# Kernel optimization log

Measured on AMD Instinct MI355X. Metric: run time of the kernel, lower is better.

The kernel has to match this reference:

```python
import jax, jax.numpy as jnp
import numpy as np

B, S, D = 2, 2048, 1024
H, HD = 16, 64          # n_heads, head_dim
FF, HID = 4096, 8192    # d_ff, swiglu hidden (= 2*d_ff)


def _ln(x, eps=1e-5):
    # non-parametric LayerNorm (fp8_layernorm_noparam in source)
    m = jnp.mean(x, axis=-1, keepdims=True)
    v = jnp.var(x, axis=-1, keepdims=True)
    return (x - m) * jax.lax.rsqrt(v + eps)


def setup_inputs() -> dict:
    key = jax.random.key(0)
    ks = jax.random.split(key, 7)
    s = 0.02  # init std
    return {
        "x": jax.random.normal(ks[0], (B, S, D), jnp.float32),
        "Wq": jax.random.normal(ks[1], (D, D), jnp.float32) * s,
        "Wk": jax.random.normal(ks[2], (D, D), jnp.float32) * s,
        "Wv": jax.random.normal(ks[3], (D, D), jnp.float32) * s,
        "Wo": jax.random.normal(ks[4], (D, D), jnp.float32) * s,
        "Wff": jax.random.normal(ks[5], (HID, D), jnp.float32) * s,
        "Wout": jax.random.normal(ks[6], (FF, D), jnp.float32).T * s,  # [D, FF] -> stored as Linear weight [D_out=D, D_in=FF]
    }


def reference(x, Wq, Wk, Wv, Wo, Wff, Wout):
    b, s, d = x.shape
    # attention sub-block
    h = _ln(x)
    q = (h @ Wq.T).reshape(b, s, H, HD).transpose(0, 2, 1, 3)  # [B,H,S,HD]
    k = (h @ Wk.T).reshape(b, s, H, HD).transpose(0, 2, 1, 3)
    v = (h @ Wv.T).reshape(b, s, H, HD).transpose(0, 2, 1, 3)
    scale = 1.0 / float(HD) ** 0.5
    scores = jnp.einsum('bhqd,bhkd->bhqk', q, k) * scale        # [B,H,S,S] naive full matrix
    causal = jnp.tril(jnp.ones((s, s), dtype=bool))
    scores = jnp.where(causal, scores, jnp.finfo(scores.dtype).min)
    attn = jax.nn.softmax(scores, axis=-1)
    att = jnp.einsum('bhqk,bhkd->bhqd', attn, v)                # [B,H,S,HD]
    att = att.transpose(0, 2, 1, 3).reshape(b, s, d)
    x = x + att @ Wo.T
    # MLP sub-block (SwiGLU, OLMo Llama-style)
    h2 = _ln(x)
    ff = h2 @ Wff.T                                             # [B,S,HID]
    x1, x2 = jnp.split(ff, 2, axis=-1)
    g = jax.nn.silu(x1) * x2                                    # [B,S,FF]
    return x + g @ Wout.T
```

## Files before the change

### kernel.cpp

```cpp
#include <hip/hip_runtime.h>
#include <hip/hip_bf16.h>

#define B_ 2
#define S_ 2048
#define D_ 1024
#define H_ 16
#define FF_ 4096
#define M_ (B_*S_)

using u16 = unsigned short;
using u32 = unsigned int;
typedef __attribute__((ext_vector_type(8))) short short8;
typedef __attribute__((ext_vector_type(4))) float f32x4;
typedef __attribute__((ext_vector_type(16))) float f32x16;
typedef __attribute__((ext_vector_type(4))) unsigned short u16x4;
typedef __attribute__((ext_vector_type(4))) unsigned int u32x4;

static __device__ __forceinline__ u16 f2bf(float f) {
  __hip_bfloat16 h = __float2bfloat16(f);
  return *reinterpret_cast<u16*>(&h);
}
static __device__ __forceinline__ float bf2f(u16 u) {
  __hip_bfloat16 h; *reinterpret_cast<u16*>(&h) = u;
  return __bfloat162float(h);
}

#define GLDS(gp, lp) __builtin_amdgcn_global_load_lds( \
    (const __attribute__((address_space(1))) void*)(gp), \
    (__attribute__((address_space(3))) void*)(lp), 16, 0, 0)

#define MFMA16(a, b, c) __builtin_amdgcn_mfma_f32_16x16x32_bf16(a, b, c, 0, 0, 0)
#define VMC(n) asm volatile("s_waitcnt vmcnt(" #n ")" ::: "memory")
#define BAR() __builtin_amdgcn_s_barrier()

__global__ __launch_bounds__(256) void conv_f32_bf16(
    const float* __restrict__ src, u16* __restrict__ dst, int n4) {
  int i = blockIdx.x * 256 + threadIdx.x;
  if (i < n4) {
    float4 v = reinterpret_cast<const float4*>(src)[i];
    u16x4 o;
    o.x = f2bf(v.x); o.y = f2bf(v.y); o.z = f2bf(v.z); o.w = f2bf(v.w);
    reinterpret_cast<u16x4*>(dst)[i] = o;
  }
}

__global__ __launch_bounds__(256) void ln_rows(
    const float* __restrict__ x, u16* __restrict__ out) {
  int row = blockIdx.x;
  int t = threadIdx.x;
  float4 v = reinterpret_cast<const float4*>(x + (size_t)row * D_)[t];
  float s  = v.x + v.y + v.z + v.w;
  float ss = v.x*v.x + v.y*v.y + v.z*v.z + v.w*v.w;
  #pragma unroll
  for (int off = 1; off < 64; off <<= 1) {
    s  += __shfl_xor(s,  off, 64);
    ss += __shfl_xor(ss, off, 64);
  }
  __shared__ float rs[4], rss[4];
  int wid = t >> 6;
  if ((t & 63) == 0) { rs[wid] = s; rss[wid] = ss; }
  __syncthreads();
  s  = rs[0] + rs[1] + rs[2] + rs[3];
  ss = rss[0] + rss[1] + rss[2] + rss[3];
  float mean = s * (1.0f / D_);
  float var  = ss * (1.0f / D_) - mean * mean;
  float r = rsqrtf(var + 1e-5f);
  u16x4 o;
  o.x = f2bf((v.x - mean) * r);
  o.y = f2bf((v.y - mean) * r);
  o.z = f2bf((v.z - mean) * r);
  o.w = f2bf((v.w - mean) * r);
  reinterpret_cast<u16x4*>(out + (size_t)row * D_)[t] = o;
}

template<int MODE>
__global__ __launch_bounds__(256, 2) void gemm_bt2(
    const u16* __restrict__ A, const u16* __restrict__ W,
    void* __restrict__ C, const u16* __restrict__ aux,
    const float* __restrict__ res, int M, int N, int K)
{
  __shared__ u16 lds[32768];
  const int tid = threadIdx.x;
  const int wid = tid >> 6, lane = tid & 63;
  const int g = lane >> 4, c = lane & 15;
  const int gridN = N >> 7;
  int nwg = gridDim.x;
  int lin = blockIdx.x;
  lin = (lin & 7) * (nwg >> 3) + (lin >> 3);
  const int bm = lin / gridN, bn = lin % gridN;
  const int wm = wid >> 1, wn = wid & 1;
  const int NT = K >> 6;

  f32x4 acc[4][4];
  #pragma unroll
  for (int i = 0; i < 4; i++)
    #pragma unroll
    for (int j = 0; j < 4; j++) acc[i][j] = {0.f, 0.f, 0.f, 0.f};

  auto stage = [&](int sel, int t) {
    const u16* src = sel ? W : A;
    const int tilerow = (sel ? bn : bm) * 128;
    char* dst = (char*)&lds[sel * 16384 + (t & 1) * 8192];
    #pragma unroll
    for (int i = 0; i < 4; i++) {
      int j = i * 256 + tid;
      int row = j >> 3, col16 = j & 7;
      const u16* gp = src + (size_t)(tilerow + row) * K + t * 64 + ((col16 ^ (row & 7)) << 3);
      GLDS(gp, dst + j * 16);
    }
  };

  stage(0, 0); stage(1, 0);
  __syncthreads();

  for (int t = 0; t < NT; t++) {
    const int buf = t & 1;
    if (t + 1 < NT) { stage(0, t + 1); stage(1, t + 1); }

    short8 af[2][4], bfr[2][4];
    #pragma unroll
    for (int ks = 0; ks < 2; ks++)
      #pragma unroll
      for (int m = 0; m < 4; m++) {
        int rh = wm * 64 + m * 16 + c;
        af[ks][m] = *reinterpret_cast<const short8*>(
            &lds[buf * 8192 + rh * 64 + ((((ks << 2) | g) ^ (rh & 7)) << 3)]);
      }
    #pragma unroll
    for (int ks = 0; ks < 2; ks++)
      #pragma unroll
      for (int n = 0; n < 4; n++) {
        int rh = wn * 64 + n * 16 + c;
        bfr[ks][n] = *reinterpret_cast<const short8*>(
            &lds[16384 + buf * 8192 + rh * 64 + ((((ks << 2) | g) ^ (rh & 7)) << 3)]);
      }
    __builtin_amdgcn_s_setprio(1);
    #pragma unroll
    for (int m = 0; m < 4; m++)
      #pragma unroll
      for (int n = 0; n < 4; n++) {
        acc[m][n] = MFMA16(af[0][m], bfr[0][n], acc[m][n]);
        acc[m][n] = MFMA16(af[1][m], bfr[1][n], acc[m][n]);
      }
    __builtin_amdgcn_s_setprio(0);
    __syncthreads();
  }

  #pragma unroll
  for (int m = 0; m < 4; m++)
    #pragma unroll
    for (int n = 0; n < 4; n++)
      #pragma unroll
      for (int r = 0; r < 4; r++) {
        int gr = bm * 128 + wm * 64 + m * 16 + g * 4 + r;
        int gc = bn * 128 + wn * 64 + n * 16 + c;
        size_t idx = (size_t)gr * N + gc;
        float v = acc[m][n][r];
        if (MODE == 0) {
          ((u16*)C)[idx] = f2bf(v);
        } else if (MODE == 1) {
          ((float*)C)[idx] = v + res[idx];
        }
      }
}

__global__ __launch_bounds__(256, 2) void gemm_ff(
    const u16* __restrict__ A, const u16* __restrict__ W,
    u16* __restrict__ Cout, int M, int N, int K)
{
  __shared__ u16 lds[24576];
  const int tid = threadIdx.x;
  const int wid = tid >> 6, lane = tid & 63;
  const int g = lane >> 4, c = lane & 15;
  const int gridN = N >> 7;
  int nwg = gridDim.x;
  int lin = blockIdx.x;
  lin = (lin & 7) * (nwg >> 3) + (lin >> 3);
  const int bm = lin / gridN, bn = lin % gridN;
  const int wm = wid >> 1, wn = wid & 1;
  const int NT = K >> 5;

  f32x4 ac1[4][4], ac2[4][4];
  #pragma unroll
  for (int i = 0; i < 4; i++)
    #pragma unroll
    for (int j = 0; j < 4; j++) { ac1[i][j] = {0.f,0.f,0.f,0.f}; ac2[i][j] = {0.f,0.f,0.f,0.f}; }

  auto stage = [&](int sel, int t) {
    const u16* src = (sel == 0) ? A : W;
    const int rowbase = (sel == 0) ? bm * 128 : (sel == 1 ? bn * 128 : 4096 + bn * 128);
    char* dst = (char*)&lds[sel * 8192 + (t & 1) * 4096];
    #pragma unroll
    for (int i = 0; i < 2; i++) {
      int j = i * 256 + tid;
      int r = j >> 2, cslot = j & 3;
      int csrc = cslot ^ ((r >> 1) & 3);
      const u16* gp = src + (size_t)(rowbase + r) * K + t * 32 + csrc * 8;
      GLDS(gp, dst + j * 16);
    }
  };

  stage(0, 0); stage(1, 0); stage(2, 0);
  __syncthreads();

  for (int t = 0; t < NT; t++) {
    const int buf = t & 1;
    if (t + 1 < NT) { stage(0, t + 1); stage(1, t + 1); stage(2, t + 1); }

    short8 af[4], b1f[4], b2f[4];
    #pragma unroll
    for (int m = 0; m < 4; m++) {
      int rh = wm * 64 + m * 16 + c;
      af[m] = *reinterpret_cast<const short8*>(
          &lds[buf * 4096 + rh * 32 + ((g ^ ((rh >> 1) & 3)) << 3)]);
    }
    #pragma unroll
    for (int n = 0; n < 4; n++) {
      int rh = wn * 64 + n * 16 + c;
      b1f[n] = *reinterpret_cast<const short8*>(
          &lds[8192 + buf * 4096 + rh * 32 + ((g ^ ((rh >> 1) & 3)) << 3)]);
      b2f[n] = *reinterpret_cast<const short8*>(
          &lds[16384 + buf * 4096 + rh * 32 + ((g ^ ((rh >> 1) & 3)) << 3)]);
    }
    __builtin_amdgcn_s_setprio(1);
    #pragma unroll
    for (int m = 0; m < 4; m++)
      #pragma unroll
      for (int n = 0; n < 4; n++) {
        ac1[m][n] = MFMA16(af[m], b1f[n], ac1[m][n]);
        ac2[m][n] = MFMA16(af[m], b2f[n], ac2[m][n]);
      }
    __builtin_amdgcn_s_setprio(0);
    __syncthreads();
  }

  #pragma unroll
  for (int m = 0; m < 4; m++)
    #pragma unroll
    for (int n = 0; n < 4; n++)
      #pragma unroll
      for (int r = 0; r < 4; r++) {
        int gr = bm * 128 + wm * 64 + m * 16 + g * 4 + r;
        int gc = bn * 128 + wn * 64 + n * 16 + c;
        float v1 = ac1[m][n][r];
        float v2 = ac2[m][n][r];
        float gv = (v1 / (1.0f + __expf(-v1))) * v2;
        Cout[(size_t)gr * N + gc] = f2bf(gv);
      }
}

__global__ __launch_bounds__(256) void transpose_v(
    const u16* __restrict__ qkv, u16* __restrict__ vT) {
  __shared__ u16 t[64][66];
  int bh = blockIdx.y;
  int s0 = blockIdx.x * 64;
  int b = bh >> 4, h = bh & 15;
  int tid = threadIdx.x;
  #pragma unroll
  for (int it = 0; it < 2; it++) {
    int idx = it * 256 + tid;
    int row = idx >> 3;
    int cc  = (idx & 7) * 8;
    const u16* src = qkv + ((size_t)(b * S_ + s0 + row)) * 3072 + 2048 + h * 64 + cc;
    short8 v = *reinterpret_cast<const short8*>(src);
    #pragma unroll
    for (int j = 0; j < 8; j++) t[row][cc + j] = (u16)v[j];
  }
  __syncthreads();
  #pragma unroll
  for (int it = 0; it < 2; it++) {
    int idx = it * 256 + tid;
    int d  = idx >> 3;
    int sc = (idx & 7) * 8;
    short8 o;
    #pragma unroll
    for (int j = 0; j < 8; j++) o[j] = (short)t[sc + j][d];
    *reinterpret_cast<short8*>(vT + ((size_t)bh * 64 + d) * S_ + s0 + sc) = o;
  }
}

__global__ __launch_bounds__(256) void attn_split(
    const u16* __restrict__ qkv, const u16* __restrict__ vT,
    u16* __restrict__ pO, float* __restrict__ pML) {
  __shared__ u16 Kl[2][2048];
  __shared__ u16 Vl[2][2048];
  const int tid  = threadIdx.x;
  const int lane = tid & 63;
  const int wid  = tid >> 6;
  const int l31  = lane & 31;
  const int half = lane >> 5;

  int lin = blockIdx.x;
  int swz = (lin & 7) * 160 + (lin >> 3);
  int bh  = swz / 40;
  int j   = swz - bh * 40;
  int qq = 15, rem = j;
  while (rem > (qq >> 2)) { rem -= (qq >> 2) + 1; qq--; }
  int ci = rem;
  const int qt  = qq * 4 + wid;
  const int kt0 = ci * 16;
  const int nt  = min(qq * 4 + 3, kt0 + 15) - kt0;
  int ubase = (qt < 16) ? qt : (qt < 32) ? 16 + (qt - 16) * 2 + ci
            : (qt < 48) ? 48 + (qt - 32) * 3 + ci : 96 + (qt - 48) * 4 + ci;
  const int punit = bh * 160 + ubase;

  const int b = bh >> 4, hd = bh & 15;
  const int q_base = qt * 32;

  const u16* Qb = qkv + ((size_t)(b * S_ + q_base + l31)) * 3072 + hd * 64;
  const u16* Kb = qkv + (size_t)b * S_ * 3072 + 1024 + hd * 64;
  const u16* Vt = vT + (size_t)bh * 64 * S_;

  short8 qf[4];
  #pragma unroll
  for (int dt = 0; dt < 4; dt++) {
    short8 v = *reinterpret_cast<const short8*>(Qb + dt * 16 + half * 8);
    #pragma unroll
    for (int jj = 0; jj < 8; jj++) v[jj] = (short)f2bf(bf2f((u16)v[jj]) * 0.18033688f);
    qf[dt] = v;
  }

  auto stageKV = [&](int kt, int buf) {
    {
      int row = tid >> 3, cs = tid & 7;
      int c = cs ^ (row & 7);
      const u16* gp = Kb + (size_t)(kt * 32 + row) * 3072 + c * 8;
      GLDS(gp, (char*)&Kl[buf][0] + tid * 16);
    }
    {
      int row = tid >> 2, cs = tid & 3;
      int c = cs ^ (row & 3);
      const u16* gp = Vt + (size_t)row * S_ + kt * 32 + c * 8;
      GLDS(gp, (char*)&Vl[buf][0] + tid * 16);
    }
  };

  f32x16 o0, o1;
  #pragma unroll
  for (int r = 0; r < 16; r++) { o0[r] = 0.f; o1[r] = 0.f; }
  float m = -1e30f, lsum = 0.f;

  stageKV(kt0, 0);
  VMC(0); BAR();

  for (int i = 0; ; i++) {
    const int kt = kt0 + i;
    const int buf = i & 1;
    if (i < nt) stageKV(kt + 1, buf ^ 1);

    if (kt <= qt) {
      const bool diag = (kt == qt);
      short8 kfr[4], vfr[4];
      #pragma unroll
      for (int dt = 0; dt < 4; dt++) {
        int cs = (dt * 2 + half) ^ (l31 & 7);
        kfr[dt] = *reinterpret_cast<const short8*>((const char*)&Kl[buf][0] + l31 * 128 + cs * 16);
      }
      {
        int r0 = l31, r1 = 32 + l31;
        vfr[0] = *reinterpret_cast<const short8*>((const char*)&Vl[buf][0] + r0 * 64 + ((half       ^ (r0 & 3)) * 16));
        vfr[1] = *reinterpret_cast<const short8*>((const char*)&Vl[buf][0] + r0 * 64 + (((2 + half) ^ (r0 & 3)) * 16));
        vfr[2] = *reinterpret_cast<const short8*>((const char*)&Vl[buf][0] + r1 * 64 + ((half       ^ (r1 & 3)) * 16));
        vfr[3] = *reinterpret_cast<const short8*>((const char*)&Vl[buf][0] + r1 * 64 + (((2 + half) ^ (r1 & 3)) * 16));
      }

      f32x16 s;
      #pragma unroll
      for (int r = 0; r < 16; r++) s[r] = 0.f;
      __builtin_amdgcn_s_setprio(1);
      #pragma unroll
      for (int dt = 0; dt < 4; dt++)
        s = __builtin_amdgcn_mfma_f32_32x32x16_bf16(kfr[dt], qf[dt], s, 0, 0, 0);
      __builtin_amdgcn_s_setprio(0);

      float p[16];
      #pragma unroll
      for (int r = 0; r < 16; r++) {
        p[r] = s[r];
        if (diag) {
          int kloc = half * 4 + (r & 3) + 8 * (r >> 2);
          if (kloc > l31) p[r] = -1e30f;
        }
      }
      float t8[8];
      #pragma unroll
      for (int r = 0; r < 8; r++) t8[r] = fmaxf(p[r], p[r + 8]);
      float t4a = fmaxf(t8[0], t8[4]), t4b = fmaxf(t8[1], t8[5]);
      float t4c = fmaxf(t8[2], t8[6]), t4d = fmaxf(t8[3], t8[7]);
      float rm = fmaxf(fmaxf(t4a, t4b), fmaxf(t4c, t4d));
      rm = fmaxf(rm, __shfl_xor(rm, 32, 64));

      if (__any(rm > m + 11.0f)) {
        float mn = fmaxf(m, rm);
        float alpha = exp2f(m - mn);
        m = mn;
        lsum *= alpha;
        #pragma unroll
        for (int r = 0; r < 16; r++) {
          int row = (r & 3) + 8 * (r >> 2) + 4 * half;
          float ar = __shfl(alpha, row, 64);
          o0[r] *= ar; o1[r] *= ar;
        }
      }
      float rs = 0.f;
      #pragma unroll
      for (int r = 0; r < 16; r++) { p[r] = exp2f(p[r] - m); rs += p[r]; }
      rs += __shfl_xor(rs, 32, 64);
      lsum += rs;

      u32 pk[8], sp[8];
      #pragma unroll
      for (int ii = 0; ii < 8; ii++) {
        pk[ii] = (u32)f2bf(p[2 * ii]) | ((u32)f2bf(p[2 * ii + 1]) << 16);
        sp[ii] = (u32)__shfl_xor((int)pk[ii], 32, 64);
      }
      u32x4 a0 = { half ? sp[2] : pk[0], half ? sp[3] : pk[1],
                   half ? pk[2] : sp[0], half ? pk[3] : sp[1] };
      u32x4 a1 = { half ? sp[6] : pk[4], half ? sp[7] : pk[5],
                   half ? pk[6] : sp[4], half ? pk[7] : sp[5] };
      short8 pa0 = *reinterpret_cast<short8*>(&a0);
      short8 pa1 = *reinterpret_cast<short8*>(&a1);

      __builtin_amdgcn_s_setprio(1);
      o0 = __builtin_amdgcn_mfma_f32_32x32x16_bf16(pa0, vfr[0], o0, 0, 0, 0);
      o0 = __builtin_amdgcn_mfma_f32_32x32x16_bf16(pa1, vfr[1], o0, 0, 0, 0);
      o1 = __builtin_amdgcn_mfma_f32_32x32x16_bf16(pa0, vfr[2], o1, 0, 0, 0);
      o1 = __builtin_amdgcn_mfma_f32_32x32x16_bf16(pa1, vfr[3], o1, 0, 0, 0);
      __builtin_amdgcn_s_setprio(0);
    }

    if (i == nt) break;
    VMC(0); BAR();
  }

  #pragma unroll
  for (int r = 0; r < 16; r++) {
    int row = (r & 3) + 8 * (r >> 2) + 4 * half;
    pO[(size_t)punit * 2048 + row * 64 + l31]      = f2bf(o0[r]);
    pO[(size_t)punit * 2048 + row * 64 + 32 + l31] = f2bf(o1[r]);
  }
  if (half == 0) {
    pML[punit * 64 + l31]      = m;
    pML[punit * 64 + 32 + l31] = lsum;
  }
}

__global__ __launch_bounds__(256) void attn_combine(
    const u16* __restrict__ pO, const float* __restrict__ pML,
    u16* __restrict__ att) {
  int gw = blockIdx.x;
  int bh = gw >> 6, qt = gw & 63;
  int b = bh >> 4, hd = bh & 15;
  int nc = (qt >> 4) + 1;
  int base = (qt < 16) ? qt : (qt < 32) ? 16 + (qt - 16) * 2
           : (qt < 48) ? 48 + (qt - 32) * 3 : 96 + (qt - 48) * 4;
  int p0 = bh * 160 + base;
  int q  = threadIdx.x >> 3;
  int d  = (threadIdx.x & 7) * 8;

  float m0 = pML[p0 * 64 + q];
  float l0 = pML[p0 * 64 + 32 + q];
  float m1 = nc > 1 ? pML[(p0 + 1) * 64 + q]      : -1e30f;
  float l1 = nc > 1 ? pML[(p0 + 1) * 64 + 32 + q] : 0.f;
  float m2 = nc > 2 ? pML[(p0 + 2) * 64 + q]      : -1e30f;
  float l2 = nc > 2 ? pML[(p0 + 2) * 64 + 32 + q] : 0.f;
  float m3 = nc > 3 ? pML[(p0 + 3) * 64 + q]      : -1e30f;
  float l3 = nc > 3 ? pML[(p0 + 3) * 64 + 32 + q] : 0.f;
  float M = fmaxf(fmaxf(m0, m1), fmaxf(m2, m3));
  float w0 = exp2f(m0 - M), w1 = exp2f(m1 - M);
  float w2 = exp2f(m2 - M), w3 = exp2f(m3 - M);
  float L = l0 * w0 + l1 * w1 + l2 * w2 + l3 * w3;
  float invL = 1.0f / L;

  float o[8];
  short8 v0 = *reinterpret_cast<const short8*>(&pO[(size_t)p0 * 2048 + q * 64 + d]);
  #pragma unroll
  for (int jj = 0; jj < 8; jj++) o[jj] = bf2f((u16)v0[jj]) * w0;
  if (nc > 1) {
    short8 v = *reinterpret_cast<const short8*>(&pO[(size_t)(p0 + 1) * 2048 + q * 64 + d]);
    #pragma unroll
    for (int jj = 0; jj < 8; jj++) o[jj] += bf2f((u16)v[jj]) * w1;
  }
  if (nc > 2) {
    short8 v = *reinterpret_cast<const short8*>(&pO[(size_t)(p0 + 2) * 2048 + q * 64 + d]);
    #pragma unroll
    for (int jj = 0; jj < 8; jj++) o[jj] += bf2f((u16)v[jj]) * w2;
  }
  if (nc > 3) {
    short8 v = *reinterpret_cast<const short8*>(&pO[(size_t)(p0 + 3) * 2048 + q * 64 + d]);
    #pragma unroll
    for (int jj = 0; jj < 8; jj++) o[jj] += bf2f((u16)v[jj]) * w3;
  }
  short8 ov;
  #pragma unroll
  for (int jj = 0; jj < 8; jj++) ov[jj] = (short)f2bf(o[jj] * invL);
  *reinterpret_cast<short8*>(
      &att[((size_t)(b * S_ + qt * 32 + q)) * D_ + hd * 64 + d]) = ov;
}

extern "C" void kernel_launch(void* const* d_in, const int* in_sizes, int n_in,
                              void* d_out, int out_size, void* d_ws, size_t ws_size,
                              hipStream_t stream) {
  (void)in_sizes; (void)n_in; (void)out_size; (void)ws_size;
  const float* x    = (const float*)d_in[0];
  const float* Wq   = (const float*)d_in[1];
  const float* Wk   = (const float*)d_in[2];
  const float* Wv   = (const float*)d_in[3];
  const float* Wo   = (const float*)d_in[4];
  const float* Wff  = (const float*)d_in[5];
  const float* Wout = (const float*)d_in[6];
  float* out = (float*)d_out;

  char* ws = (char*)d_ws;
  u16*   wqkv = (u16*)(ws);
  u16*   wo   = (u16*)(ws + 6291456);
  u16*   wff  = (u16*)(ws + 8388608);
  u16*   wout = (u16*)(ws + 25165824);
  float* x1   = (float*)(ws + 33554432);
  char*  P    = ws + 50331648;
  u16*   hbuf = (u16*)(P);
  u16*   qkv  = (u16*)(P + 8388608);
  u16*   vT   = (u16*)(P + 33554432);
  u16*   att  = (u16*)(P + 41943040);
  u16*   pO   = (u16*)(P + 50331648);
  float* pML  = (float*)(P + 71303168);
  u16*   h2   = (u16*)(P);
  u16*   gbuf = (u16*)(P + 41943040);

  conv_f32_bf16<<<1024, 256, 0, stream>>>(Wq, wqkv,               262144);
  conv_f32_bf16<<<1024, 256, 0, stream>>>(Wk, wqkv + 1048576,     262144);
  conv_f32_bf16<<<1024, 256, 0, stream>>>(Wv, wqkv + 2097152,     262144);
  conv_f32_bf16<<<1024, 256, 0, stream>>>(Wo, wo,                 262144);
  conv_f32_bf16<<<8192, 256, 0, stream>>>(Wff, wff,               2097152);
  conv_f32_bf16<<<4096, 256, 0, stream>>>(Wout, wout,             1048576);

  ln_rows<<<M_, 256, 0, stream>>>(x, hbuf);
  gemm_bt2<0><<<dim3(768), 256, 0, stream>>>(hbuf, wqkv, qkv, nullptr, nullptr, M_, 3072, 1024);
  transpose_v<<<dim3(32, 32), 256, 0, stream>>>(qkv, vT);
  attn_split<<<dim3(1280), 256, 0, stream>>>(qkv, vT, pO, pML);
  attn_combine<<<dim3(2048), 256, 0, stream>>>(pO, pML, att);
  gemm_bt2<1><<<dim3(256), 256, 0, stream>>>(att, wo, x1, nullptr, x, M_, 1024, 1024);

  ln_rows<<<M_, 256, 0, stream>>>(x1, h2);
  gemm_ff<<<dim3(1024), 256, 0, stream>>>(h2, wff, gbuf, M_, 4096, 1024);
  gemm_bt2<1><<<dim3(256), 256, 0, stream>>>(gbuf, wout, out, nullptr, x1, M_, 1024, 4096);
}
```

Baseline: 281.8 us.

## Triple-buffer GEMM pipelines with single barrier and smaller M tiles for N=1024 GEMMs

After: 298.1 us. 1.06x slower.

```diff
diff --git a/kernel.cpp b/kernel.cpp
--- a/kernel.cpp
+++ b/kernel.cpp
@@ -32,6 +32,7 @@
 #define MFMA16(a, b, c) __builtin_amdgcn_mfma_f32_16x16x32_bf16(a, b, c, 0, 0, 0)
 #define VMC(n) asm volatile("s_waitcnt vmcnt(" #n ")" ::: "memory")
 #define BAR() __builtin_amdgcn_s_barrier()
+#define CFENCE() asm volatile("" ::: "memory")
 
 __global__ __launch_bounds__(256) void conv_f32_bf16(
     const float* __restrict__ src, u16* __restrict__ dst, int n4) {
@@ -73,102 +74,12 @@
   reinterpret_cast<u16x4*>(out + (size_t)row * D_)[t] = o;
 }
 
-template<int MODE>
-__global__ __launch_bounds__(256, 2) void gemm_bt2(
+template<int MODE, int MB>
+__global__ __launch_bounds__(256, 3) void gemm_bt3(
     const u16* __restrict__ A, const u16* __restrict__ W,
-    void* __restrict__ C, const u16* __restrict__ aux,
-    const float* __restrict__ res, int M, int N, int K)
+    void* __restrict__ C, const float* __restrict__ res, int M, int N, int K)
 {
-  __shared__ u16 lds[32768];
-  const int tid = threadIdx.x;
-  const int wid = tid >> 6, lane = tid & 63;
-  const int g = lane >> 4, c = lane & 15;
-  const int gridN = N >> 7;
-  int nwg = gridDim.x;
-  int lin = blockIdx.x;
-  lin = (lin & 7) * (nwg >> 3) + (lin >> 3);
-  const int bm = lin / gridN, bn = lin % gridN;
-  const int wm = wid >> 1, wn = wid & 1;
-  const int NT = K >> 6;
-
-  f32x4 acc[4][4];
-  #pragma unroll
-  for (int i = 0; i < 4; i++)
-    #pragma unroll
-    for (int j = 0; j < 4; j++) acc[i][j] = {0.f, 0.f, 0.f, 0.f};
-
-  auto stage = [&](int sel, int t) {
-    const u16* src = sel ? W : A;
-    const int tilerow = (sel ? bn : bm) * 128;
-    char* dst = (char*)&lds[sel * 16384 + (t & 1) * 8192];
-    #pragma unroll
-    for (int i = 0; i < 4; i++) {
-      int j = i * 256 + tid;
-      int row = j >> 3, col16 = j & 7;
-      const u16* gp = src + (size_t)(tilerow + row) * K + t * 64 + ((col16 ^ (row & 7)) << 3);
-      GLDS(gp, dst + j * 16);
-    }
-  };
-
-  stage(0, 0); stage(1, 0);
-  __syncthreads();
-
-  for (int t = 0; t < NT; t++) {
-    const int buf = t & 1;
-    if (t + 1 < NT) { stage(0, t + 1); stage(1, t + 1); }
-
-    short8 af[2][4], bfr[2][4];
-    #pragma unroll
-    for (int ks = 0; ks < 2; ks++)
-      #pragma unroll
-      for (int m = 0; m < 4; m++) {
-        int rh = wm * 64 + m * 16 + c;
-        af[ks][m] = *reinterpret_cast<const short8*>(
-            &lds[buf * 8192 + rh * 64 + ((((ks << 2) | g) ^ (rh & 7)) << 3)]);
-      }
-    #pragma unroll
-    for (int ks = 0; ks < 2; ks++)
-      #pragma unroll
-      for (int n = 0; n < 4; n++) {
-        int rh = wn * 64 + n * 16 + c;
-        bfr[ks][n] = *reinterpret_cast<const short8*>(
-            &lds[16384 + buf * 8192 + rh * 64 + ((((ks << 2) | g) ^ (rh & 7)) << 3)]);
-      }
-    __builtin_amdgcn_s_setprio(1);
-    #pragma unroll
-    for (int m = 0; m < 4; m++)
-      #pragma unroll
-      for (int n = 0; n < 4; n++) {
-        acc[m][n] = MFMA16(af[0][m], bfr[0][n], acc[m][n]);
-        acc[m][n] = MFMA16(af[1][m], bfr[1][n], acc[m][n]);
-      }
-    __builtin_amdgcn_s_setprio(0);
-    __syncthreads();
-  }
-
-  #pragma unroll
-  for (int m = 0; m < 4; m++)
-    #pragma unroll
-    for (int n = 0; n < 4; n++)
-      #pragma unroll
-      for (int r = 0; r < 4; r++) {
-        int gr = bm * 128 + wm * 64 + m * 16 + g * 4 + r;
-        int gc = bn * 128 + wn * 64 + n * 16 + c;
-        size_t idx = (size_t)gr * N + gc;
-        float v = acc[m][n][r];
-        if (MODE == 0) {
-          ((u16*)C)[idx] = f2bf(v);
-        } else if (MODE == 1) {
-          ((float*)C)[idx] = v + res[idx];
-        }
-      }
-}
-
-__global__ __launch_bounds__(256, 2) void gemm_ff(
-    const u16* __restrict__ A, const u16* __restrict__ W,
-    u16* __restrict__ Cout, int M, int N, int K)
-{
-  __shared__ u16 lds[24576];
+  __shared__ u16 lds[MB * 96 + 12288];
   const int tid = threadIdx.x;
   const int wid = tid >> 6, lane = tid & 63;
   const int g = lane >> 4, c = lane & 15;
@@ -180,33 +91,127 @@
   const int wm = wid >> 1, wn = wid & 1;
   const int NT = K >> 5;
 
-  f32x4 ac1[4][4], ac2[4][4];
-  #pragma unroll
-  for (int i = 0; i < 4; i++)
-    #pragma unroll
-    for (int j = 0; j < 4; j++) { ac1[i][j] = {0.f,0.f,0.f,0.f}; ac2[i][j] = {0.f,0.f,0.f,0.f}; }
-
-  auto stage = [&](int sel, int t) {
-    const u16* src = (sel == 0) ? A : W;
-    const int rowbase = (sel == 0) ? bm * 128 : (sel == 1 ? bn * 128 : 4096 + bn * 128);
-    char* dst = (char*)&lds[sel * 8192 + (t & 1) * 4096];
+  f32x4 acc[MB / 32][4];
+  #pragma unroll
+  for (int i = 0; i < MB / 32; i++)
+    #pragma unroll
+    for (int j = 0; j < 4; j++) acc[i][j] = {0.f, 0.f, 0.f, 0.f};
+
+  auto stage = [&](int t) {
+    #pragma unroll
+    for (int i = 0; i < MB / 64; i++) {
+      int j = i * 256 + tid;
+      int r = j >> 2, cslot = j & 3;
+      const u16* gp = A + (size_t)(bm * MB + r) * K + t * 32 + ((cslot ^ ((r >> 1) & 3)) * 8);
+      GLDS(gp, (char*)&lds[(t % 3) * MB * 32] + j * 16);
+    }
     #pragma unroll
     for (int i = 0; i < 2; i++) {
       int j = i * 256 + tid;
       int r = j >> 2, cslot = j & 3;
-      int csrc = cslot ^ ((r >> 1) & 3);
-      const u16* gp = src + (size_t)(rowbase + r) * K + t * 32 + csrc * 8;
-      GLDS(gp, dst + j * 16);
+      const u16* gp = W + (size_t)(bn * 128 + r) * K + t * 32 + ((cslot ^ ((r >> 1) & 3)) * 8);
+      GLDS(gp, (char*)&lds[MB * 96 + (t % 3) * 4096] + j * 16);
     }
   };
 
-  stage(0, 0); stage(1, 0); stage(2, 0);
-  __syncthreads();
+  stage(0); stage(1);
 
   for (int t = 0; t < NT; t++) {
-    const int buf = t & 1;
-    if (t + 1 < NT) { stage(0, t + 1); stage(1, t + 1); stage(2, t + 1); }
-
+    if (t + 1 < NT) {
+      if constexpr (MB == 128) { VMC(4); } else { VMC(3); }
+    } else {
+      VMC(0);
+    }
+    BAR(); CFENCE();
+    if (t + 2 < NT) stage(t + 2);
+
+    const int buf = t % 3;
+    short8 af[MB / 32], bfr[4];
+    #pragma unroll
+    for (int m = 0; m < MB / 32; m++) {
+      int rh = wm * (MB / 2) + m * 16 + c;
+      af[m] = *reinterpret_cast<const short8*>(
+          &lds[buf * MB * 32 + rh * 32 + ((g ^ ((rh >> 1) & 3)) << 3)]);
+    }
+    #pragma unroll
+    for (int n = 0; n < 4; n++) {
+      int rh = wn * 64 + n * 16 + c;
+      bfr[n] = *reinterpret_cast<const short8*>(
+          &lds[MB * 96 + buf * 4096 + rh * 32 + ((g ^ ((rh >> 1) & 3)) << 3)]);
+    }
+    __builtin_amdgcn_s_setprio(1);
+    #pragma unroll
+    for (int m = 0; m < MB / 32; m++)
+      #pragma unroll
+      for (int n = 0; n < 4; n++)
+        acc[m][n] = MFMA16(af[m], bfr[n], acc[m][n]);
+    __builtin_amdgcn_s_setprio(0);
+  }
+
+  #pragma unroll
+  for (int m = 0; m < MB / 32; m++)
+    #pragma unroll
+    for (int n = 0; n < 4; n++)
+      #pragma unroll
+      for (int r = 0; r < 4; r++) {
+        int gr = bm * MB + wm * (MB / 2) + m * 16 + g * 4 + r;
+        int gc = bn * 128 + wn * 64 + n * 16 + c;
+        size_t idx = (size_t)gr * N + gc;
+        float v = acc[m][n][r];
+        if (MODE == 0) {
+          ((u16*)C)[idx] = f2bf(v);
+        } else {
+          ((float*)C)[idx] = v + res[idx];
+        }
+      }
+}
+
+__global__ __launch_bounds__(256, 2) void gemm_ff(
+    const u16* __restrict__ A, const u16* __restrict__ W,
+    u16* __restrict__ Cout, int M, int N, int K)
+{
+  __shared__ u16 lds[36864];
+  const int tid = threadIdx.x;
+  const int wid = tid >> 6, lane = tid & 63;
+  const int g = lane >> 4, c = lane & 15;
+  const int gridN = N >> 7;
+  int nwg = gridDim.x;
+  int lin = blockIdx.x;
+  lin = (lin & 7) * (nwg >> 3) + (lin >> 3);
+  const int bm = lin / gridN, bn = lin % gridN;
+  const int wm = wid >> 1, wn = wid & 1;
+  const int NT = K >> 5;
+
+  f32x4 ac1[4][4], ac2[4][4];
+  #pragma unroll
+  for (int i = 0; i < 4; i++)
+    #pragma unroll
+    for (int j = 0; j < 4; j++) { ac1[i][j] = {0.f,0.f,0.f,0.f}; ac2[i][j] = {0.f,0.f,0.f,0.f}; }
+
+  auto stage = [&](int t) {
+    #pragma unroll
+    for (int sel = 0; sel < 3; sel++) {
+      const u16* src = (sel == 0) ? A : W;
+      const int rowbase = (sel == 0) ? bm * 128 : (sel == 1 ? bn * 128 : 4096 + bn * 128);
+      char* dst = (char*)&lds[sel * 12288 + (t % 3) * 4096];
+      #pragma unroll
+      for (int i = 0; i < 2; i++) {
+        int j = i * 256 + tid;
+        int r = j >> 2, cslot = j & 3;
+        const u16* gp = src + (size_t)(rowbase + r) * K + t * 32 + ((cslot ^ ((r >> 1) & 3)) * 8);
+        GLDS(gp, dst + j * 16);
+      }
+    }
+  };
+
+  stage(0); stage(1);
+
+  for (int t = 0; t < NT; t++) {
+    if (t + 1 < NT) { VMC(6); } else { VMC(0); }
+    BAR(); CFENCE();
+    if (t + 2 < NT) stage(t + 2);
+
+    const int buf = t % 3;
     short8 af[4], b1f[4], b2f[4];
     #pragma unroll
     for (int m = 0; m < 4; m++) {
@@ -218,9 +223,9 @@
     for (int n = 0; n < 4; n++) {
       int rh = wn * 64 + n * 16 + c;
       b1f[n] = *reinterpret_cast<const short8*>(
-          &lds[8192 + buf * 4096 + rh * 32 + ((g ^ ((rh >> 1) & 3)) << 3)]);
+          &lds[12288 + buf * 4096 + rh * 32 + ((g ^ ((rh >> 1) & 3)) << 3)]);
       b2f[n] = *reinterpret_cast<const short8*>(
-          &lds[16384 + buf * 4096 + rh * 32 + ((g ^ ((rh >> 1) & 3)) << 3)]);
+          &lds[24576 + buf * 4096 + rh * 32 + ((g ^ ((rh >> 1) & 3)) << 3)]);
     }
     __builtin_amdgcn_s_setprio(1);
     #pragma unroll
@@ -231,7 +236,6 @@
         ac2[m][n] = MFMA16(af[m], b2f[n], ac2[m][n]);
       }
     __builtin_amdgcn_s_setprio(0);
-    __syncthreads();
   }
 
   #pragma unroll
@@ -535,13 +539,13 @@
   conv_f32_bf16<<<4096, 256, 0, stream>>>(Wout, wout,             1048576);
 
   ln_rows<<<M_, 256, 0, stream>>>(x, hbuf);
-  gemm_bt2<0><<<dim3(768), 256, 0, stream>>>(hbuf, wqkv, qkv, nullptr, nullptr, M_, 3072, 1024);
+  gemm_bt3<0, 128><<<dim3(768), 256, 0, stream>>>(hbuf, wqkv, qkv, nullptr, M_, 3072, 1024);
   transpose_v<<<dim3(32, 32), 256, 0, stream>>>(qkv, vT);
   attn_split<<<dim3(1280), 256, 0, stream>>>(qkv, vT, pO, pML);
   attn_combine<<<dim3(2048), 256, 0, stream>>>(pO, pML, att);
-  gemm_bt2<1><<<dim3(256), 256, 0, stream>>>(att, wo, x1, nullptr, x, M_, 1024, 1024);
+  gemm_bt3<1, 64><<<dim3(512), 256, 0, stream>>>(att, wo, x1, x, M_, 1024, 1024);
 
   ln_rows<<<M_, 256, 0, stream>>>(x1, h2);
   gemm_ff<<<dim3(1024), 256, 0, stream>>>(h2, wff, gbuf, M_, 4096, 1024);
-  gemm_bt2<1><<<dim3(256), 256, 0, stream>>>(gbuf, wout, out, nullptr, x1, M_, 1024, 4096);
-}
+  gemm_bt3<1, 64><<<dim3(512), 256, 0, stream>>>(gbuf, wout, out, x1, M_, 1024, 4096);
+}
```

## Triple-buffer LDS staging in SwiGLU GEMM and attention with single barrier

Applied to the files above, without the earlier changes.

Result: no change. 286.3 us (+1.6%).

```diff
diff --git a/kernel.cpp b/kernel.cpp
--- a/kernel.cpp
+++ b/kernel.cpp
@@ -32,6 +32,7 @@
 #define MFMA16(a, b, c) __builtin_amdgcn_mfma_f32_16x16x32_bf16(a, b, c, 0, 0, 0)
 #define VMC(n) asm volatile("s_waitcnt vmcnt(" #n ")" ::: "memory")
 #define BAR() __builtin_amdgcn_s_barrier()
+#define CFENCE() asm volatile("" ::: "memory")
 
 __global__ __launch_bounds__(256) void conv_f32_bf16(
     const float* __restrict__ src, u16* __restrict__ dst, int n4) {
@@ -76,8 +77,7 @@
 template<int MODE>
 __global__ __launch_bounds__(256, 2) void gemm_bt2(
     const u16* __restrict__ A, const u16* __restrict__ W,
-    void* __restrict__ C, const u16* __restrict__ aux,
-    const float* __restrict__ res, int M, int N, int K)
+    void* __restrict__ C, const float* __restrict__ res, int M, int N, int K)
 {
   __shared__ u16 lds[32768];
   const int tid = threadIdx.x;
@@ -158,7 +158,7 @@
         float v = acc[m][n][r];
         if (MODE == 0) {
           ((u16*)C)[idx] = f2bf(v);
-        } else if (MODE == 1) {
+        } else {
           ((float*)C)[idx] = v + res[idx];
         }
       }
@@ -168,7 +168,7 @@
     const u16* __restrict__ A, const u16* __restrict__ W,
     u16* __restrict__ Cout, int M, int N, int K)
 {
-  __shared__ u16 lds[24576];
+  __shared__ u16 lds[36864];
   const int tid = threadIdx.x;
   const int wid = tid >> 6, lane = tid & 63;
   const int g = lane >> 4, c = lane & 15;
@@ -186,27 +186,30 @@
     #pragma unroll
     for (int j = 0; j < 4; j++) { ac1[i][j] = {0.f,0.f,0.f,0.f}; ac2[i][j] = {0.f,0.f,0.f,0.f}; }
 
-  auto stage = [&](int sel, int t) {
-    const u16* src = (sel == 0) ? A : W;
-    const int rowbase = (sel == 0) ? bm * 128 : (sel == 1 ? bn * 128 : 4096 + bn * 128);
-    char* dst = (char*)&lds[sel * 8192 + (t & 1) * 4096];
-    #pragma unroll
-    for (int i = 0; i < 2; i++) {
-      int j = i * 256 + tid;
-      int r = j >> 2, cslot = j & 3;
-      int csrc = cslot ^ ((r >> 1) & 3);
-      const u16* gp = src + (size_t)(rowbase + r) * K + t * 32 + csrc * 8;
-      GLDS(gp, dst + j * 16);
+  auto stage = [&](int t) {
+    #pragma unroll
+    for (int sel = 0; sel < 3; sel++) {
+      const u16* src = (sel == 0) ? A : W;
+      const int rowbase = (sel == 0) ? bm * 128 : (sel == 1 ? bn * 128 : 4096 + bn * 128);
+      char* dst = (char*)&lds[sel * 12288 + (t % 3) * 4096];
+      #pragma unroll
+      for (int i = 0; i < 2; i++) {
+        int j = i * 256 + tid;
+        int r = j >> 2, cslot = j & 3;
+        const u16* gp = src + (size_t)(rowbase + r) * K + t * 32 + ((cslot ^ ((r >> 1) & 3)) * 8);
+        GLDS(gp, dst + j * 16);
+      }
     }
   };
 
-  stage(0, 0); stage(1, 0); stage(2, 0);
-  __syncthreads();
+  stage(0); stage(1);
 
   for (int t = 0; t < NT; t++) {
-    const int buf = t & 1;
-    if (t + 1 < NT) { stage(0, t + 1); stage(1, t + 1); stage(2, t + 1); }
-
+    if (t + 1 < NT) { VMC(6); } else { VMC(0); }
+    BAR(); CFENCE();
+    if (t + 2 < NT) stage(t + 2);
+
+    const int buf = t % 3;
     short8 af[4], b1f[4], b2f[4];
     #pragma unroll
     for (int m = 0; m < 4; m++) {
@@ -218,9 +221,9 @@
     for (int n = 0; n < 4; n++) {
       int rh = wn * 64 + n * 16 + c;
       b1f[n] = *reinterpret_cast<const short8*>(
-          &lds[8192 + buf * 4096 + rh * 32 + ((g ^ ((rh >> 1) & 3)) << 3)]);
+          &lds[12288 + buf * 4096 + rh * 32 + ((g ^ ((rh >> 1) & 3)) << 3)]);
       b2f[n] = *reinterpret_cast<const short8*>(
-          &lds[16384 + buf * 4096 + rh * 32 + ((g ^ ((rh >> 1) & 3)) << 3)]);
+          &lds[24576 + buf * 4096 + rh * 32 + ((g ^ ((rh >> 1) & 3)) << 3)]);
     }
     __builtin_amdgcn_s_setprio(1);
     #pragma unroll
@@ -231,7 +234,6 @@
         ac2[m][n] = MFMA16(af[m], b2f[n], ac2[m][n]);
       }
     __builtin_amdgcn_s_setprio(0);
-    __syncthreads();
   }
 
   #pragma unroll
@@ -282,8 +284,8 @@
 __global__ __launch_bounds__(256) void attn_split(
     const u16* __restrict__ qkv, const u16* __restrict__ vT,
     u16* __restrict__ pO, float* __restrict__ pML) {
-  __shared__ u16 Kl[2][2048];
-  __shared__ u16 Vl[2][2048];
+  __shared__ u16 Kl[3][2048];
+  __shared__ u16 Vl[3][2048];
   const int tid  = threadIdx.x;
   const int lane = tid & 63;
   const int wid  = tid >> 6;
@@ -329,7 +331,7 @@
     }
     {
       int row = tid >> 2, cs = tid & 3;
-      int c = cs ^ (row & 3);
+      int c = cs ^ ((row >> 1) & 3);
       const u16* gp = Vt + (size_t)row * S_ + kt * 32 + c * 8;
       GLDS(gp, (char*)&Vl[buf][0] + tid * 16);
     }
@@ -341,12 +343,13 @@
   float m = -1e30f, lsum = 0.f;
 
   stageKV(kt0, 0);
-  VMC(0); BAR();
+  if (nt >= 1) { stageKV(kt0 + 1, 1); VMC(2); } else { VMC(0); }
+  BAR();
 
   for (int i = 0; ; i++) {
     const int kt = kt0 + i;
-    const int buf = i & 1;
-    if (i < nt) stageKV(kt + 1, buf ^ 1);
+    const int buf = i % 3;
+    if (i + 2 <= nt) stageKV(kt0 + i + 2, (i + 2) % 3);
 
     if (kt <= qt) {
       const bool diag = (kt == qt);
@@ -358,10 +361,11 @@
       }
       {
         int r0 = l31, r1 = 32 + l31;
-        vfr[0] = *reinterpret_cast<const short8*>((const char*)&Vl[buf][0] + r0 * 64 + ((half       ^ (r0 & 3)) * 16));
-        vfr[1] = *reinterpret_cast<const short8*>((const char*)&Vl[buf][0] + r0 * 64 + (((2 + half) ^ (r0 & 3)) * 16));
-        vfr[2] = *reinterpret_cast<const short8*>((const char*)&Vl[buf][0] + r1 * 64 + ((half       ^ (r1 & 3)) * 16));
-        vfr[3] = *reinterpret_cast<const short8*>((const char*)&Vl[buf][0] + r1 * 64 + (((2 + half) ^ (r1 & 3)) * 16));
+        int x0 = (r0 >> 1) & 3, x1 = (r1 >> 1) & 3;
+        vfr[0] = *reinterpret_cast<const short8*>((const char*)&Vl[buf][0] + r0 * 64 + ((half       ^ x0) * 16));
+        vfr[1] = *reinterpret_cast<const short8*>((const char*)&Vl[buf][0] + r0 * 64 + (((2 + half) ^ x0) * 16));
+        vfr[2] = *reinterpret_cast<const short8*>((const char*)&Vl[buf][0] + r1 * 64 + ((half       ^ x1) * 16));
+        vfr[3] = *reinterpret_cast<const short8*>((const char*)&Vl[buf][0] + r1 * 64 + (((2 + half) ^ x1) * 16));
       }
 
       f32x16 s;
@@ -430,7 +434,8 @@
     }
 
     if (i == nt) break;
-    VMC(0); BAR();
+    if (i + 2 <= nt) { VMC(2); } else { VMC(0); }
+    BAR();
   }
 
   #pragma unroll
@@ -535,13 +540,13 @@
   conv_f32_bf16<<<4096, 256, 0, stream>>>(Wout, wout,             1048576);
 
   ln_rows<<<M_, 256, 0, stream>>>(x, hbuf);
-  gemm_bt2<0><<<dim3(768), 256, 0, stream>>>(hbuf, wqkv, qkv, nullptr, nullptr, M_, 3072, 1024);
+  gemm_bt2<0><<<dim3(768), 256, 0, stream>>>(hbuf, wqkv, qkv, nullptr, M_, 3072, 1024);
   transpose_v<<<dim3(32, 32), 256, 0, stream>>>(qkv, vT);
   attn_split<<<dim3(1280), 256, 0, stream>>>(qkv, vT, pO, pML);
   attn_combine<<<dim3(2048), 256, 0, stream>>>(pO, pML, att);
-  gemm_bt2<1><<<dim3(256), 256, 0, stream>>>(att, wo, x1, nullptr, x, M_, 1024, 1024);
+  gemm_bt2<1><<<dim3(256), 256, 0, stream>>>(att, wo, x1, x, M_, 1024, 1024);
 
   ln_rows<<<M_, 256, 0, stream>>>(x1, h2);
   gemm_ff<<<dim3(1024), 256, 0, stream>>>(h2, wff, gbuf, M_, 4096, 1024);
-  gemm_bt2<1><<<dim3(256), 256, 0, stream>>>(gbuf, wout, out, nullptr, x1, M_, 1024, 4096);
-}
+  gemm_bt2<1><<<dim3(256), 256, 0, stream>>>(gbuf, wout, out, x1, M_, 1024, 4096);
+}
```
